# Kernel tuning notes

Measured on AMD Instinct MI355X. Metric: run time of the kernel, lower is better.

The kernel has to match this reference:

```python
import jax, jax.numpy as jnp
import numpy as np

B, L, H, V, HALF = 128, 4096, 64, 64, 32
ALPHA = 0.95
LN_EPS = 1e-5


def _normalize(x):
    # torch F.normalize(dim=-1): x / max(||x||_2, 1e-12)
    n = jnp.linalg.norm(x, axis=-1, keepdims=True)
    return x / jnp.maximum(n, 1e-12)


def setup_inputs() -> dict:
    key = jax.random.key(0)
    ks = jax.random.split(key, 17)
    s = 0.05
    return {
        "seq": jax.random.randint(ks[0], (B, L), 0, V),
        "embed": jax.random.normal(ks[1], (V, H), jnp.float32),
        "W1": jax.random.normal(ks[2], (H, 2 * H), jnp.float32) * s,
        "b1": jnp.zeros((2 * H,), jnp.float32),
        "W2": jax.random.normal(ks[3], (2 * H, H), jnp.float32) * s,
        "b2": jnp.zeros((H,), jnp.float32),
        "gamma": jnp.ones((H,), jnp.float32),
        "beta": jnp.zeros((H,), jnp.float32),
        "Ws": jax.random.normal(ks[4], (H, HALF), jnp.float32) * s,
        "bs": jnp.zeros((HALF,), jnp.float32),
        "We": jax.random.normal(ks[5], (H, HALF), jnp.float32) * s,
        "be": jnp.zeros((HALF,), jnp.float32),
        "Wrp": jax.random.normal(ks[6], (2 * HALF, H), jnp.float32) * s,
        "brp": jnp.zeros((H,), jnp.float32),
        "Wout": jax.random.normal(ks[7], (H, V), jnp.float32) * s,
        "bout": jnp.zeros((V,), jnp.float32),
    }


def _forward(seq, embed, W1, b1, W2, b2, gamma, beta,
             Ws, bs, We, be, Wrp, brp, Wout, bout):
    # Encoder: embed + FF(ReLU) residual + LayerNorm
    h0 = embed[seq]                                   # [B,L,H]
    ff = jnp.maximum(h0 @ W1 + b1, 0.0) @ W2 + b2
    x = h0 + ff
    mu = x.mean(-1, keepdims=True)
    var = ((x - mu) ** 2).mean(-1, keepdims=True)
    h = (x - mu) / jnp.sqrt(var + LN_EPS) * gamma + beta  # [B,L,H]

    # Precompute per-step projections for t = 0 .. L-2
    hp = h[:, :-1, :]                                 # [B,L-1,H]
    hs = hp @ Ws + bs                                 # [B,L-1,HALF]
    he = hp @ We + be
    ksn = _normalize(hs)
    ken = _normalize(he)
    scale = (jnp.arange(L - 1, dtype=h.dtype) + 1.0) / L  # (t+1)/L

    def step(carry, inp):
        M_s, M_e = carry                              # [B,HALF,HALF]
        hs_t, he_t, ks_t, ke_t, sc = inp
        vps = jnp.einsum('bij,bj->bi', M_s, ks_t)
        vpe = jnp.einsum('bij,bj->bi', M_e, ke_t)
        M_s = M_s + (1.0 - ALPHA) * (hs_t - vps)[:, :, None] * ks_t[:, None, :]
        M_e = M_e + (1.0 - ALPHA) * sc * (he_t - vpe)[:, :, None] * ke_t[:, None, :]
        return (M_s, M_e), None

    xs = (jnp.swapaxes(hs, 0, 1), jnp.swapaxes(he, 0, 1),
          jnp.swapaxes(ksn, 0, 1), jnp.swapaxes(ken, 0, 1), scale)
    M0 = jnp.zeros((B, HALF, HALF), h.dtype)
    (M_s, M_e), _ = jax.lax.scan(step, (M0, M0), xs)

    # Read with last-token query
    q = h[:, -1, :]
    qs = _normalize(q @ Ws + bs)
    qe = _normalize(q @ We + be)
    rs = jnp.einsum('bij,bj->bi', M_s, qs)
    re = jnp.einsum('bij,bj->bi', M_e, qe)
    r = jnp.concatenate([rs, re], axis=-1)            # [B,2*HALF]
    return (r @ Wrp + brp) @ Wout + bout              # [B,V]


def reference(seq, embed, W1, b1, W2, b2, gamma, beta,
              Ws, bs, We, be, Wrp, brp, Wout, bout):
    return _forward(seq, embed, W1, b1, W2, b2, gamma, beta,
                    Ws, bs, We, be, Wrp, brp, Wout, bout)
```

## Files before the change

kernel.cpp:

```cpp
#include <hip/hip_runtime.h>
#include <hip/hip_bf16.h>
#include <stdint.h>


#define BETA 0.05f
#define NB 128
#define NL 4096
#define TC 16
#define NCH 256
#define NBLD 6
#define RCH 24
#define SLOT_F 336
#define NSLOT 48

#define L_GR   (NSLOT * SLOT_F)
#define L_DA   (L_GR + 4096)
#define L_RV   (L_DA + 64)
#define L_O1   (L_RV + 64)
#define L_WHO  (L_O1 + 64)
#define L_TOT  (L_WHO + 1)

struct Ptrs { const void* p[15]; };

__device__ inline float readlane_f(float v, int l) {
    return __int_as_float(__builtin_amdgcn_readlane(__float_as_int(v), l));
}
__device__ inline float ldT(const float* p, int i) { return p[i]; }
__device__ inline float ldT(const __hip_bfloat16* p, int i) { return __bfloat162float(p[i]); }

template <typename T>
__device__ void build_tables_body(const T* emb, const T* W1, const T* b1,
                                  const T* W2, const T* b2, const T* gam,
                                  const T* bet, const T* Wsm, const T* bsv,
                                  const T* Wem, const T* bev, float* tbl)
{
    int v = blockIdx.x;
    int j = threadIdx.x;
    __shared__ float h0s[64];
    __shared__ float act[128];
    __shared__ float hrow[64];

    float h0 = ldT(emb, v * 64 + j);
    h0s[j] = h0;
    __syncthreads();

    float za = ldT(b1, j);
    float zb = ldT(b1, j + 64);
    for (int k = 0; k < 64; ++k) {
        float hk = h0s[k];
        za = fmaf(hk, ldT(W1, k * 128 + j), za);
        zb = fmaf(hk, ldT(W1, k * 128 + j + 64), zb);
    }
    act[j] = fmaxf(za, 0.0f);
    act[j + 64] = fmaxf(zb, 0.0f);
    __syncthreads();

    float ff = ldT(b2, j);
    for (int k = 0; k < 128; ++k)
        ff = fmaf(act[k], ldT(W2, k * 64 + j), ff);
    float x = h0 + ff;

    float s = x;
    for (int off = 32; off >= 1; off >>= 1) s += __shfl_xor(s, off, 64);
    float mu = s * (1.0f / 64.0f);
    float d = x - mu;
    float s2 = d * d;
    for (int off = 32; off >= 1; off >>= 1) s2 += __shfl_xor(s2, off, 64);
    float var = s2 * (1.0f / 64.0f);
    float h = d / sqrtf(var + 1e-5f) * ldT(gam, j) + ldT(bet, j);
    hrow[j] = h;
    __syncthreads();

    if (j < 32) {
        float sv = ldT(bsv, j);
        for (int k = 0; k < 64; ++k)
            sv = fmaf(hrow[k], ldT(Wsm, k * 32 + j), sv);
        float n2 = sv * sv;
        for (int off = 16; off >= 1; off >>= 1) n2 += __shfl_xor(n2, off, 64);
        float nrm = fmaxf(sqrtf(n2), 1e-12f);
        tbl[v * 32 + j] = sv;
        tbl[2048 + v * 32 + j] = sv / nrm;
    } else {
        int jj = j - 32;
        float ev = ldT(bev, jj);
        for (int k = 0; k < 64; ++k)
            ev = fmaf(hrow[k], ldT(Wem, k * 32 + jj), ev);
        float n2 = ev * ev;
        for (int off = 16; off >= 1; off >>= 1) n2 += __shfl_xor(n2, off, 64);
        float nrm = fmaxf(sqrtf(n2), 1e-12f);
        tbl[4096 + v * 32 + jj] = ev;
        tbl[6144 + v * 32 + jj] = ev / nrm;
    }
}

__global__ __launch_bounds__(64, 2) void build_tables(Ptrs ps, float* __restrict__ tbl,
                                                      int* __restrict__ flags)
{
    if (blockIdx.x == 0) {
        flags[threadIdx.x] = 0;
        flags[threadIdx.x + 64] = 0;
    }
    uint32_t g0 = *(const uint32_t*)ps.p[5];
    if (g0 == 0x3F803F80u)
        build_tables_body((const __hip_bfloat16*)ps.p[0], (const __hip_bfloat16*)ps.p[1],
                          (const __hip_bfloat16*)ps.p[2], (const __hip_bfloat16*)ps.p[3],
                          (const __hip_bfloat16*)ps.p[4], (const __hip_bfloat16*)ps.p[5],
                          (const __hip_bfloat16*)ps.p[6], (const __hip_bfloat16*)ps.p[7],
                          (const __hip_bfloat16*)ps.p[8], (const __hip_bfloat16*)ps.p[9],
                          (const __hip_bfloat16*)ps.p[10], tbl);
    else
        build_tables_body((const float*)ps.p[0], (const float*)ps.p[1],
                          (const float*)ps.p[2], (const float*)ps.p[3],
                          (const float*)ps.p[4], (const float*)ps.p[5],
                          (const float*)ps.p[6], (const float*)ps.p[7],
                          (const float*)ps.p[8], (const float*)ps.p[9],
                          (const float*)ps.p[10], tbl);
}

__global__ __launch_bounds__(512, 1) void ema_ms(
    const int* __restrict__ seq, const float* __restrict__ tbl,
    Ptrs ps, float* __restrict__ rvbuf, int* __restrict__ flags,
    void* __restrict__ outv)
{
    __shared__ __align__(16) float S[L_TOT];

    int bm = blockIdx.x;
    int b = bm >> 1, mat = bm & 1;
    int tid = threadIdx.x;
    int wid = tid >> 6, lane = tid & 63;
    const float bstep = BETA / 4096.0f;

    if (tid < 64) S[L_DA + tid] = 0.0f;

    const float* ktab = tbl + 2048 + mat * 4096;
    for (int i = tid; i < 2048; i += 512)
        S[(i >> 5) * 33 + (i & 31)] = ktab[i];
    __syncthreads();

    {
        float Kown[32];
#pragma unroll
        for (int j = 0; j < 32; ++j) Kown[j] = S[lane * 33 + j];
        for (int v8 = 0; v8 < 8; ++v8) {
            int vt = wid * 8 + v8;
            float acc = 0.0f;
#pragma unroll
            for (int j = 0; j < 32; ++j)
                acc = fmaf(S[vt * 33 + j], Kown[j], acc);
            S[L_GR + vt * 64 + lane] = acc;
        }
    }
    __syncthreads();

    const int* sb = seq + (size_t)b * NL;
    float y = 0.0f;
    if (wid == 0) {
        int vlast = sb[NL - 1];
        y = S[L_GR + vlast * 64 + lane];
    }

    const int NRND = (NCH + RCH - 1) / RCH;

    for (int r = 0; r <= NRND; ++r) {
        if (wid != 0 && wid != 4) {
            int bi = (wid > 4) ? (wid - 2) : (wid - 1);
            if (r < NRND) {
                int g = lane >> 4, q = lane & 15;
                int ci = RCH * r + 4 * bi + g;
                int valid = (ci < NCH);
                int cic = valid ? ci : (NCH - 1);
                int c = NCH - 1 - cic;
                float* slot = S + ((r & 1) * RCH + 4 * bi + g) * SLOT_F;
                int t = c * TC + (TC - 1) - q;
                int tokv = sb[t];
                float bb = mat ? bstep * (float)(t + 1) : BETA;
                if (t == NL - 1) bb = 0.0f;
                float bneg = -bb;
                if (valid) ((int*)(slot + 320))[q] = tokv;

                float garr[TC];
#pragma unroll
                for (int p = 0; p < TC; ++p) {
                    int vp = __shfl(tokv, p, 16);
                    garr[p] = S[L_GR + vp * 64 + tokv] * bneg;
                }
                float x[TC];
                x[0] = (q == 0) ? 1.0f : 0.0f;
#pragma unroll
                for (int p = 1; p < TC; ++p) {
                    float t0 = 0.f, t1 = 0.f, t2 = 0.f, t3 = 0.f;
#pragma unroll
                    for (int j2 = 0; j2 < p; ++j2) {
                        float cpj = __shfl(garr[p], j2, 16);
                        if ((j2 & 3) == 0)      t0 = fmaf(cpj, x[j2], t0);
                        else if ((j2 & 3) == 1) t1 = fmaf(cpj, x[j2], t1);
                        else if ((j2 & 3) == 2) t2 = fmaf(cpj, x[j2], t2);
                        else                    t3 = fmaf(cpj, x[j2], t3);
                    }
                    x[p] = ((q == p) ? 1.0f : 0.0f) + ((t0 + t1) + (t2 + t3));
                }
                if (valid) {
#pragma unroll
                    for (int p = 0; p < TC; ++p)
                        slot[p * 20 + q] = x[p];
                }
            }
        } else if (wid == 0 && r >= 1) {
            int rpar = ((r - 1) & 1) * RCH;
            int base_ci = RCH * (r - 1);
            int nch_r = NCH - base_ci;
            if (nch_r > RCH) nch_r = RCH;
            int l15 = lane & 15;

            int tokr[RCH];
#pragma unroll
            for (int j = 0; j < RCH; ++j)
                tokr[j] = ((int*)(S + (rpar + j) * SLOT_F + 320))[l15];

            int stok[2][16];
            float gp[2][16];
            float4 V[2][4];
#pragma unroll
            for (int j = 0; j < 2; ++j) {
#pragma unroll
                for (int q = 0; q < 16; ++q)
                    stok[j][q] = __builtin_amdgcn_readlane(tokr[j], q);
                const float4* vr = (const float4*)(S + (rpar + j) * SLOT_F + l15 * 20);
#pragma unroll
                for (int k = 0; k < 4; ++k) V[j][k] = vr[k];
#pragma unroll
                for (int p = 0; p < 16; ++p)
                    gp[j][p] = S[L_GR + stok[j][p] * 64 + lane];
            }
            asm volatile("" ::: "memory");

#pragma unroll
            for (int jj = 0; jj < RCH; ++jj) {
                const int pb = jj & 1;
                if (jj < nch_r) {
                    int c = NCH - 1 - (base_ci + jj);
                    float bv = 0.0f;
                    if (lane < TC) {
                        int t = c * TC + (TC - 1) - lane;
                        float bb = mat ? bstep * (float)(t + 1) : BETA;
                        if (t == NL - 1) bb = 0.0f;
                        bv = bb;
                    }
                    float ryq[16];
#pragma unroll
                    for (int q = 0; q < 16; ++q)
                        ryq[q] = readlane_f(y, stok[pb][q]);
                    float s0 = V[pb][0].x * ryq[0];
                    float s1 = V[pb][0].y * ryq[1];
                    float s2 = V[pb][0].z * ryq[2];
                    float s3 = V[pb][0].w * ryq[3];
                    s0 = fmaf(V[pb][1].x, ryq[4], s0);
                    s1 = fmaf(V[pb][1].y, ryq[5], s1);
                    s2 = fmaf(V[pb][1].z, ryq[6], s2);
                    s3 = fmaf(V[pb][1].w, ryq[7], s3);
                    s0 = fmaf(V[pb][2].x, ryq[8], s0);
                    s1 = fmaf(V[pb][2].y, ryq[9], s1);
                    s2 = fmaf(V[pb][2].z, ryq[10], s2);
                    s3 = fmaf(V[pb][2].w, ryq[11], s3);
                    s0 = fmaf(V[pb][3].x, ryq[12], s0);
                    s1 = fmaf(V[pb][3].y, ryq[13], s1);
                    s2 = fmaf(V[pb][3].z, ryq[14], s2);
                    s3 = fmaf(V[pb][3].w, ryq[15], s3);
                    float dv = ((s0 + s1) + (s2 + s3)) * bv;
                    float dn = -dv;
                    float ya = 0.f, yb = 0.f, yc2 = 0.f, yd = 0.f;
#pragma unroll
                    for (int p = 0; p < TC; p += 4) {
                        ya  = fmaf(readlane_f(dn, p),     gp[pb][p],     ya);
                        yb  = fmaf(readlane_f(dn, p + 1), gp[pb][p + 1], yb);
                        yc2 = fmaf(readlane_f(dn, p + 2), gp[pb][p + 2], yc2);
                        yd  = fmaf(readlane_f(dn, p + 3), gp[pb][p + 3], yd);
                    }
                    y += (ya + yb) + (yc2 + yd);
                    if (lane < TC) atomicAdd(&S[L_DA + tokr[jj]], dv);
                }
                if (jj + 2 < RCH) {
                    const int j2 = jj + 2;
#pragma unroll
                    for (int q = 0; q < 16; ++q)
                        stok[pb][q] = __builtin_amdgcn_readlane(tokr[j2], q);
                    const float4* vr = (const float4*)(S + (rpar + j2) * SLOT_F + l15 * 20);
#pragma unroll
                    for (int k = 0; k < 4; ++k) V[pb][k] = vr[k];
#pragma unroll
                    for (int p = 0; p < 16; ++p)
                        gp[pb][p] = S[L_GR + stok[pb][p] * 64 + lane];
                }
                asm volatile("" ::: "memory");
            }
        }
        __syncthreads();
    }

    if (tid < 32) {
        float rr = 0.0f;
        const float* hsrc = tbl + mat * 4096;
        for (int v = 0; v < 64; ++v)
            rr = fmaf(S[L_DA + v], hsrc[v * 32 + tid], rr);
        __hip_atomic_store(&rvbuf[bm * 32 + tid], rr,
                           __ATOMIC_RELAXED, __HIP_MEMORY_SCOPE_AGENT);
    }
    __syncthreads();
    if (tid == 0) {
        int old = __hip_atomic_fetch_add(&flags[b], 1,
                                         __ATOMIC_ACQ_REL, __HIP_MEMORY_SCOPE_AGENT);
        ((int*)S)[L_WHO] = old;
    }
    __syncthreads();
    if (((int*)S)[L_WHO] != 1) return;

    if (tid < 64)
        S[L_RV + tid] = __hip_atomic_load(&rvbuf[b * 64 + tid],
                                          __ATOMIC_RELAXED, __HIP_MEMORY_SCOPE_AGENT);
    __syncthreads();

    uint32_t g0h = *(const uint32_t*)ps.p[5];
    int isbf = (g0h == 0x3F803F80u) ? 1 : 0;
    if (tid < 64) {
        float o;
        if (isbf) {
            const __hip_bfloat16* W = (const __hip_bfloat16*)ps.p[11];
            o = __bfloat162float(((const __hip_bfloat16*)ps.p[12])[tid]);
            for (int i = 0; i < 64; ++i)
                o = fmaf(S[L_RV + i], __bfloat162float(W[i * 64 + tid]), o);
        } else {
            const float* W = (const float*)ps.p[11];
            o = ((const float*)ps.p[12])[tid];
            for (int i = 0; i < 64; ++i)
                o = fmaf(S[L_RV + i], W[i * 64 + tid], o);
        }
        S[L_O1 + tid] = o;
    }
    __syncthreads();
    if (tid < 64) {
        float o2;
        if (isbf) {
            const __hip_bfloat16* W = (const __hip_bfloat16*)ps.p[13];
            o2 = __bfloat162float(((const __hip_bfloat16*)ps.p[14])[tid]);
            for (int i = 0; i < 64; ++i)
                o2 = fmaf(S[L_O1 + i], __bfloat162float(W[i * 64 + tid]), o2);
            ((__hip_bfloat16*)outv)[b * 64 + tid] = __float2bfloat16(o2);
        } else {
            const float* W = (const float*)ps.p[13];
            o2 = ((const float*)ps.p[14])[tid];
            for (int i = 0; i < 64; ++i)
                o2 = fmaf(S[L_O1 + i], W[i * 64 + tid], o2);
            ((float*)outv)[b * 64 + tid] = o2;
        }
    }
}

extern "C" void kernel_launch(void* const* d_in, const int* in_sizes, int n_in,
                              void* d_out, int out_size, void* d_ws, size_t ws_size,
                              hipStream_t stream) {
    const int* seq = (const int*)d_in[0];
    Ptrs ps;
    for (int i = 0; i < 15; ++i) ps.p[i] = d_in[i + 1];

    float* tbl = (float*)d_ws;
    float* rvbuf = tbl + 8192;
    int* flags = (int*)(rvbuf + 8192);

    build_tables<<<64, 64, 0, stream>>>(ps, tbl, flags);
    ema_ms<<<NB * 2, 512, 0, stream>>>(seq, tbl, ps, rvbuf, flags, d_out);
}
```

Before: 189.0 us.

## Process both memory matrices per batch in one block, drop cross-block handoff

Each block now handles both the M_s and M_e recurrences for one batch row instead of splitting them across two blocks. The serial wave-0 consumer interleaves the two independent chains, which gives it more instruction-level parallelism per step. Because both halves finish in the same block, the global atomic flag and rvbuf handoff are no longer needed. In exchange the grid is halved to 128 blocks, which leaves many CUs idle on a 256-CU part. Each block also does twice the serial work and uses more shared memory.

```diff
diff --git a/kernel.cpp b/kernel.cpp
--- a/kernel.cpp
+++ b/kernel.cpp
@@ -8,17 +8,17 @@
 #define NL 4096
 #define TC 16
 #define NCH 256
-#define NBLD 6
-#define RCH 24
+#define NSLT 512
+#define RSL 24
+#define NPAIR 12
 #define SLOT_F 336
 #define NSLOT 48
 
 #define L_GR   (NSLOT * SLOT_F)
-#define L_DA   (L_GR + 4096)
-#define L_RV   (L_DA + 64)
+#define L_DA   (L_GR + 8192)
+#define L_RV   (L_DA + 128)
 #define L_O1   (L_RV + 64)
-#define L_WHO  (L_O1 + 64)
-#define L_TOT  (L_WHO + 1)
+#define L_TOT  (L_O1 + 64)
 
 struct Ptrs { const void* p[15]; };
 
@@ -93,13 +93,8 @@
     }
 }
 
-__global__ __launch_bounds__(64, 2) void build_tables(Ptrs ps, float* __restrict__ tbl,
-                                                      int* __restrict__ flags)
+__global__ __launch_bounds__(64, 2) void build_tables(Ptrs ps, float* __restrict__ tbl)
 {
-    if (blockIdx.x == 0) {
-        flags[threadIdx.x] = 0;
-        flags[threadIdx.x + 64] = 0;
-    }
     uint32_t g0 = *(const uint32_t*)ps.p[5];
     if (g0 == 0x3F803F80u)
         build_tables_body((const __hip_bfloat16*)ps.p[0], (const __hip_bfloat16*)ps.p[1],
@@ -119,70 +114,74 @@
 
 __global__ __launch_bounds__(512, 1) void ema_ms(
     const int* __restrict__ seq, const float* __restrict__ tbl,
-    Ptrs ps, float* __restrict__ rvbuf, int* __restrict__ flags,
-    void* __restrict__ outv)
+    Ptrs ps, void* __restrict__ outv)
 {
     __shared__ __align__(16) float S[L_TOT];
 
-    int bm = blockIdx.x;
-    int b = bm >> 1, mat = bm & 1;
+    int b = blockIdx.x;
     int tid = threadIdx.x;
     int wid = tid >> 6, lane = tid & 63;
     const float bstep = BETA / 4096.0f;
-
-    if (tid < 64) S[L_DA + tid] = 0.0f;
-
-    const float* ktab = tbl + 2048 + mat * 4096;
-    for (int i = tid; i < 2048; i += 512)
-        S[(i >> 5) * 33 + (i & 31)] = ktab[i];
-    __syncthreads();
-
-    {
+    const int* sb = seq + (size_t)b * NL;
+
+    if (tid < 128) S[L_DA + tid] = 0.0f;
+
+    for (int i = tid; i < 4096; i += 512) {
+        int m = i >> 11, rest = i & 2047;
+        S[m * 2112 + (rest >> 5) * 33 + (rest & 31)] = tbl[2048 + m * 4096 + rest];
+    }
+    __syncthreads();
+
+#pragma unroll
+    for (int m = 0; m < 2; ++m) {
         float Kown[32];
 #pragma unroll
-        for (int j = 0; j < 32; ++j) Kown[j] = S[lane * 33 + j];
+        for (int j = 0; j < 32; ++j) Kown[j] = S[m * 2112 + lane * 33 + j];
         for (int v8 = 0; v8 < 8; ++v8) {
             int vt = wid * 8 + v8;
             float acc = 0.0f;
 #pragma unroll
             for (int j = 0; j < 32; ++j)
-                acc = fmaf(S[vt * 33 + j], Kown[j], acc);
-            S[L_GR + vt * 64 + lane] = acc;
+                acc = fmaf(S[m * 2112 + vt * 33 + j], Kown[j], acc);
+            S[L_GR + m * 4096 + vt * 64 + lane] = acc;
         }
     }
     __syncthreads();
 
-    const int* sb = seq + (size_t)b * NL;
-    float y = 0.0f;
+    float ym0 = 0.0f, ym1 = 0.0f;
     if (wid == 0) {
         int vlast = sb[NL - 1];
-        y = S[L_GR + vlast * 64 + lane];
-    }
-
-    const int NRND = (NCH + RCH - 1) / RCH;
+        ym0 = S[L_GR + vlast * 64 + lane];
+        ym1 = S[L_GR + 4096 + vlast * 64 + lane];
+    }
+
+    const int NRND = (NSLT + RSL - 1) / RSL;
 
     for (int r = 0; r <= NRND; ++r) {
         if (wid != 0 && wid != 4) {
             int bi = (wid > 4) ? (wid - 2) : (wid - 1);
             if (r < NRND) {
                 int g = lane >> 4, q = lane & 15;
-                int ci = RCH * r + 4 * bi + g;
-                int valid = (ci < NCH);
-                int cic = valid ? ci : (NCH - 1);
-                int c = NCH - 1 - cic;
-                float* slot = S + ((r & 1) * RCH + 4 * bi + g) * SLOT_F;
+                int s = 4 * bi + g;
+                int gi = RSL * r + s;
+                int valid = (gi < NSLT);
+                int gic = valid ? gi : (NSLT - 1);
+                int m = s & 1;
+                int c = NCH - 1 - (gic >> 1);
+                float* slot = S + ((r & 1) * RSL + s) * SLOT_F;
                 int t = c * TC + (TC - 1) - q;
                 int tokv = sb[t];
-                float bb = mat ? bstep * (float)(t + 1) : BETA;
+                float bb = m ? bstep * (float)(t + 1) : BETA;
                 if (t == NL - 1) bb = 0.0f;
                 float bneg = -bb;
                 if (valid) ((int*)(slot + 320))[q] = tokv;
 
+                const float* GB = S + L_GR + m * 4096;
                 float garr[TC];
 #pragma unroll
                 for (int p = 0; p < TC; ++p) {
                     int vp = __shfl(tokv, p, 16);
-                    garr[p] = S[L_GR + vp * 64 + tokv] * bneg;
+                    garr[p] = GB[vp * 64 + tokv] * bneg;
                 }
                 float x[TC];
                 x[0] = (q == 0) ? 1.0f : 0.0f;
@@ -206,90 +205,114 @@
                 }
             }
         } else if (wid == 0 && r >= 1) {
-            int rpar = ((r - 1) & 1) * RCH;
-            int base_ci = RCH * (r - 1);
-            int nch_r = NCH - base_ci;
-            if (nch_r > RCH) nch_r = RCH;
+            int rpar = ((r - 1) & 1) * RSL;
+            int base = RSL * (r - 1);
+            int nsl = NSLT - base;
+            if (nsl > RSL) nsl = RSL;
+            int npr = nsl >> 1;
             int l15 = lane & 15;
 
-            int tokr[RCH];
-#pragma unroll
-            for (int j = 0; j < RCH; ++j)
-                tokr[j] = ((int*)(S + (rpar + j) * SLOT_F + 320))[l15];
-
-            int stok[2][16];
-            float gp[2][16];
-            float4 V[2][4];
-#pragma unroll
-            for (int j = 0; j < 2; ++j) {
-#pragma unroll
-                for (int q = 0; q < 16; ++q)
-                    stok[j][q] = __builtin_amdgcn_readlane(tokr[j], q);
-                const float4* vr = (const float4*)(S + (rpar + j) * SLOT_F + l15 * 20);
-#pragma unroll
-                for (int k = 0; k < 4; ++k) V[j][k] = vr[k];
-#pragma unroll
-                for (int p = 0; p < 16; ++p)
-                    gp[j][p] = S[L_GR + stok[j][p] * 64 + lane];
+            int stok[2][2][16];
+            float gp[2][2][16];
+            float4 V[2][2][4];
+            int tokw[2][2];
+
+#pragma unroll
+            for (int pp = 0; pp < 2; ++pp) {
+#pragma unroll
+                for (int m = 0; m < 2; ++m) {
+                    float* sl = S + (rpar + 2 * pp + m) * SLOT_F;
+                    int tk = ((int*)(sl + 320))[l15];
+                    tokw[pp][m] = tk;
+#pragma unroll
+                    for (int q = 0; q < 16; ++q)
+                        stok[pp][m][q] = __builtin_amdgcn_readlane(tk, q);
+                    const float4* vr = (const float4*)(sl + l15 * 20);
+#pragma unroll
+                    for (int k = 0; k < 4; ++k) V[pp][m][k] = vr[k];
+#pragma unroll
+                    for (int p = 0; p < 16; ++p)
+                        gp[pp][m][p] = S[L_GR + m * 4096 + stok[pp][m][p] * 64 + lane];
+                }
             }
             asm volatile("" ::: "memory");
 
 #pragma unroll
-            for (int jj = 0; jj < RCH; ++jj) {
-                const int pb = jj & 1;
-                if (jj < nch_r) {
-                    int c = NCH - 1 - (base_ci + jj);
-                    float bv = 0.0f;
+            for (int u = 0; u < NPAIR; ++u) {
+                const int pp = u & 1;
+                if (u < npr) {
+                    int c = NCH - 1 - ((base >> 1) + u);
+                    float bv0 = 0.0f, bv1 = 0.0f;
                     if (lane < TC) {
                         int t = c * TC + (TC - 1) - lane;
-                        float bb = mat ? bstep * (float)(t + 1) : BETA;
-                        if (t == NL - 1) bb = 0.0f;
-                        bv = bb;
-                    }
-                    float ryq[16];
-#pragma unroll
-                    for (int q = 0; q < 16; ++q)
-                        ryq[q] = readlane_f(y, stok[pb][q]);
-                    float s0 = V[pb][0].x * ryq[0];
-                    float s1 = V[pb][0].y * ryq[1];
-                    float s2 = V[pb][0].z * ryq[2];
-                    float s3 = V[pb][0].w * ryq[3];
-                    s0 = fmaf(V[pb][1].x, ryq[4], s0);
-                    s1 = fmaf(V[pb][1].y, ryq[5], s1);
-                    s2 = fmaf(V[pb][1].z, ryq[6], s2);
-                    s3 = fmaf(V[pb][1].w, ryq[7], s3);
-                    s0 = fmaf(V[pb][2].x, ryq[8], s0);
-                    s1 = fmaf(V[pb][2].y, ryq[9], s1);
-                    s2 = fmaf(V[pb][2].z, ryq[10], s2);
-                    s3 = fmaf(V[pb][2].w, ryq[11], s3);
-                    s0 = fmaf(V[pb][3].x, ryq[12], s0);
-                    s1 = fmaf(V[pb][3].y, ryq[13], s1);
-                    s2 = fmaf(V[pb][3].z, ryq[14], s2);
-                    s3 = fmaf(V[pb][3].w, ryq[15], s3);
-                    float dv = ((s0 + s1) + (s2 + s3)) * bv;
-                    float dn = -dv;
-                    float ya = 0.f, yb = 0.f, yc2 = 0.f, yd = 0.f;
+                        float b0 = BETA, b1 = bstep * (float)(t + 1);
+                        if (t == NL - 1) { b0 = 0.0f; b1 = 0.0f; }
+                        bv0 = b0; bv1 = b1;
+                    }
+                    float ryq0[16], ryq1[16];
+#pragma unroll
+                    for (int q = 0; q < 16; ++q) {
+                        ryq0[q] = readlane_f(ym0, stok[pp][0][q]);
+                        ryq1[q] = readlane_f(ym1, stok[pp][1][q]);
+                    }
+                    float a0 = V[pp][0][0].x * ryq0[0];
+                    float a1 = V[pp][0][0].y * ryq0[1];
+                    float a2 = V[pp][0][0].z * ryq0[2];
+                    float a3 = V[pp][0][0].w * ryq0[3];
+                    float e0 = V[pp][1][0].x * ryq1[0];
+                    float e1 = V[pp][1][0].y * ryq1[1];
+                    float e2 = V[pp][1][0].z * ryq1[2];
+                    float e3 = V[pp][1][0].w * ryq1[3];
+#pragma unroll
+                    for (int k = 1; k < 4; ++k) {
+                        a0 = fmaf(V[pp][0][k].x, ryq0[4 * k + 0], a0);
+                        a1 = fmaf(V[pp][0][k].y, ryq0[4 * k + 1], a1);
+                        a2 = fmaf(V[pp][0][k].z, ryq0[4 * k + 2], a2);
+                        a3 = fmaf(V[pp][0][k].w, ryq0[4 * k + 3], a3);
+                        e0 = fmaf(V[pp][1][k].x, ryq1[4 * k + 0], e0);
+                        e1 = fmaf(V[pp][1][k].y, ryq1[4 * k + 1], e1);
+                        e2 = fmaf(V[pp][1][k].z, ryq1[4 * k + 2], e2);
+                        e3 = fmaf(V[pp][1][k].w, ryq1[4 * k + 3], e3);
+                    }
+                    float dv0 = ((a0 + a1) + (a2 + a3)) * bv0;
+                    float dv1 = ((e0 + e1) + (e2 + e3)) * bv1;
+                    float dn0 = -dv0, dn1 = -dv1;
+                    float p0 = 0.f, p1 = 0.f, p2 = 0.f, p3 = 0.f;
+                    float r0 = 0.f, r1 = 0.f, r2 = 0.f, r3 = 0.f;
 #pragma unroll
                     for (int p = 0; p < TC; p += 4) {
-                        ya  = fmaf(readlane_f(dn, p),     gp[pb][p],     ya);
-                        yb  = fmaf(readlane_f(dn, p + 1), gp[pb][p + 1], yb);
-                        yc2 = fmaf(readlane_f(dn, p + 2), gp[pb][p + 2], yc2);
-                        yd  = fmaf(readlane_f(dn, p + 3), gp[pb][p + 3], yd);
-                    }
-                    y += (ya + yb) + (yc2 + yd);
-                    if (lane < TC) atomicAdd(&S[L_DA + tokr[jj]], dv);
-                }
-                if (jj + 2 < RCH) {
-                    const int j2 = jj + 2;
-#pragma unroll
-                    for (int q = 0; q < 16; ++q)
-                        stok[pb][q] = __builtin_amdgcn_readlane(tokr[j2], q);
-                    const float4* vr = (const float4*)(S + (rpar + j2) * SLOT_F + l15 * 20);
-#pragma unroll
-                    for (int k = 0; k < 4; ++k) V[pb][k] = vr[k];
-#pragma unroll
-                    for (int p = 0; p < 16; ++p)
-                        gp[pb][p] = S[L_GR + stok[pb][p] * 64 + lane];
+                        p0 = fmaf(readlane_f(dn0, p),     gp[pp][0][p],     p0);
+                        p1 = fmaf(readlane_f(dn0, p + 1), gp[pp][0][p + 1], p1);
+                        p2 = fmaf(readlane_f(dn0, p + 2), gp[pp][0][p + 2], p2);
+                        p3 = fmaf(readlane_f(dn0, p + 3), gp[pp][0][p + 3], p3);
+                        r0 = fmaf(readlane_f(dn1, p),     gp[pp][1][p],     r0);
+                        r1 = fmaf(readlane_f(dn1, p + 1), gp[pp][1][p + 1], r1);
+                        r2 = fmaf(readlane_f(dn1, p + 2), gp[pp][1][p + 2], r2);
+                        r3 = fmaf(readlane_f(dn1, p + 3), gp[pp][1][p + 3], r3);
+                    }
+                    ym0 += (p0 + p1) + (p2 + p3);
+                    ym1 += (r0 + r1) + (r2 + r3);
+                    if (lane < TC) {
+                        atomicAdd(&S[L_DA + tokw[pp][0]], dv0);
+                        atomicAdd(&S[L_DA + 64 + tokw[pp][1]], dv1);
+                    }
+                }
+                if (u + 2 < npr) {
+#pragma unroll
+                    for (int m = 0; m < 2; ++m) {
+                        float* sl = S + (rpar + 2 * (u + 2) + m) * SLOT_F;
+                        int tk = ((int*)(sl + 320))[l15];
+                        tokw[pp][m] = tk;
+#pragma unroll
+                        for (int q = 0; q < 16; ++q)
+                            stok[pp][m][q] = __builtin_amdgcn_readlane(tk, q);
+                        const float4* vr = (const float4*)(sl + l15 * 20);
+#pragma unroll
+                        for (int k = 0; k < 4; ++k) V[pp][m][k] = vr[k];
+#pragma unroll
+                        for (int p = 0; p < 16; ++p)
+                            gp[pp][m][p] = S[L_GR + m * 4096 + stok[pp][m][p] * 64 + lane];
+                    }
                 }
                 asm volatile("" ::: "memory");
             }
@@ -297,26 +320,15 @@
         __syncthreads();
     }
 
-    if (tid < 32) {
+    if (tid < 64) {
+        int half = tid >> 5;
+        int j = tid & 31;
+        const float* hsrc = tbl + half * 4096;
         float rr = 0.0f;
-        const float* hsrc = tbl + mat * 4096;
         for (int v = 0; v < 64; ++v)
-            rr = fmaf(S[L_DA + v], hsrc[v * 32 + tid], rr);
-        __hip_atomic_store(&rvbuf[bm * 32 + tid], rr,
-                           __ATOMIC_RELAXED, __HIP_MEMORY_SCOPE_AGENT);
-    }
-    __syncthreads();
-    if (tid == 0) {
-        int old = __hip_atomic_fetch_add(&flags[b], 1,
-                                         __ATOMIC_ACQ_REL, __HIP_MEMORY_SCOPE_AGENT);
-        ((int*)S)[L_WHO] = old;
-    }
-    __syncthreads();
-    if (((int*)S)[L_WHO] != 1) return;
-
-    if (tid < 64)
-        S[L_RV + tid] = __hip_atomic_load(&rvbuf[b * 64 + tid],
-                                          __ATOMIC_RELAXED, __HIP_MEMORY_SCOPE_AGENT);
+            rr = fmaf(S[L_DA + half * 64 + v], hsrc[v * 32 + j], rr);
+        S[L_RV + tid] = rr;
+    }
     __syncthreads();
 
     uint32_t g0h = *(const uint32_t*)ps.p[5];
@@ -363,9 +375,7 @@
     for (int i = 0; i < 15; ++i) ps.p[i] = d_in[i + 1];
 
     float* tbl = (float*)d_ws;
-    float* rvbuf = tbl + 8192;
-    int* flags = (int*)(rvbuf + 8192);
-
-    build_tables<<<64, 64, 0, stream>>>(ps, tbl, flags);
-    ema_ms<<<NB * 2, 512, 0, stream>>>(seq, tbl, ps, rvbuf, flags, d_out);
-}
+
+    build_tables<<<64, 64, 0, stream>>>(ps, tbl);
+    ema_ms<<<NB, 512, 0, stream>>>(seq, tbl, ps, d_out);
+}
```

Result: slower. 280.3 us (+48.3%).
